# Kernel optimization log

Measured on AMD Instinct MI355X. Metric: run time of the kernel, lower is better.

The kernel has to match this reference:

```python
import jax, jax.numpy as jnp
import numpy as np

N = 50000
E = 800000
D_IN = 128
D_OUT = 128


def setup_inputs() -> dict:
    key = jax.random.key(0)
    ks = jax.random.split(key, 12)
    x = jax.random.normal(ks[0], (N, D_IN), dtype=jnp.float32)
    edge_index = jax.random.randint(ks[1], (2, E), 0, N, dtype=jnp.int64)
    importance = jax.random.uniform(ks[2], (N, 1), dtype=jnp.float32)
    s = 1.0 / np.sqrt(D_IN)
    W_msg = jax.random.uniform(ks[3], (D_IN, D_OUT), jnp.float32, -s, s)
    b_msg = jax.random.uniform(ks[4], (D_OUT,), jnp.float32, -s, s)
    s2 = 1.0 / np.sqrt(D_IN + D_OUT)
    W_upd = jax.random.uniform(ks[5], (D_IN + D_OUT, D_OUT), jnp.float32, -s2, s2)
    b_upd = jax.random.uniform(ks[6], (D_OUT,), jnp.float32, -s2, s2)
    s3 = 1.0 / np.sqrt(D_OUT + 1)
    W_gate = jax.random.uniform(ks[7], (D_OUT + 1, D_OUT), jnp.float32, -s3, s3)
    b_gate = jax.random.uniform(ks[8], (D_OUT,), jnp.float32, -s3, s3)
    s4 = 1.0 / np.sqrt(D_OUT)
    W_imp = jax.random.uniform(ks[9], (D_OUT, 1), jnp.float32, -s4, s4)
    b_imp = jax.random.uniform(ks[10], (1,), jnp.float32, -s4, s4)
    return {
        "x": x, "edge_index": edge_index, "importance": importance,
        "W_msg": W_msg, "b_msg": b_msg, "W_upd": W_upd, "b_upd": b_upd,
        "W_gate": W_gate, "b_gate": b_gate, "W_imp": W_imp, "b_imp": b_imp,
    }


def reference(x, edge_index, importance, W_msg, b_msg, W_upd, b_upd,
              W_gate, b_gate, W_imp, b_imp):
    src, dst = edge_index[0], edge_index[1]
    # message: lin_message(x_j). Transform nodes once (N < E), then gather.
    m_nodes = x @ W_msg + b_msg              # [N, D_OUT]
    msgs = m_nodes[src]                      # [E, D_OUT] gather
    aggr = jax.ops.segment_sum(msgs, dst, num_segments=N)  # [N, D_OUT] scatter-add
    # update: lin_update(cat([x, aggr]))
    conv_out = jnp.concatenate([x, aggr], axis=-1) @ W_upd + b_upd  # [N, D_OUT]
    # sigmoid-gated residual mix with importance
    gate_in = jnp.concatenate([conv_out, importance], axis=-1)      # [N, D_OUT+1]
    gate = jax.nn.sigmoid(gate_in @ W_gate + b_gate)
    out = gate * conv_out + (1.0 - gate) * x
    propagated_importance = out @ W_imp + b_imp                     # [N, 1]
    return out, propagated_importance
```

## Files before the change

kernel.cpp:

```cpp
#include <hip/hip_runtime.h>
#include <hip/hip_bf16.h>

#define D 128
#define BR 64
#define PWS 132
#define PXS 65

__global__ void count_deg(const int* __restrict__ ei, int* __restrict__ deg, int E) {
    int e = blockIdx.x * 256 + threadIdx.x;
    if (e < E) atomicAdd(&deg[ei[E + e]], 1);
}

__global__ __launch_bounds__(256) void scan_kernel(const int* __restrict__ deg,
                                                   int* __restrict__ rowstart,
                                                   int* __restrict__ cursor, int n) {
    __shared__ int tsum[257];
    int tid = threadIdx.x;
    int chunk = (n + 255) / 256;
    int lo = tid * chunk;
    int hi = lo + chunk; if (hi > n) hi = n;
    int s = 0;
    for (int i = lo; i < hi; ++i) s += deg[i];
    tsum[tid] = s;
    __syncthreads();
    if (tid == 0) {
        int run = 0;
        for (int i = 0; i < 256; ++i) { int t = tsum[i]; tsum[i] = run; run += t; }
        tsum[256] = run;
    }
    __syncthreads();
    int run = tsum[tid];
    for (int i = lo; i < hi; ++i) {
        rowstart[i] = run; cursor[i] = run; run += deg[i];
    }
    if (tid == 0) rowstart[n] = tsum[256];
}

__global__ void fill_csr(const int* __restrict__ ei, int* __restrict__ cursor,
                         int* __restrict__ csr, int E) {
    int e = blockIdx.x * 256 + threadIdx.x;
    if (e < E) {
        int s = ei[e];
        int d = ei[E + e];
        int p = atomicAdd(&cursor[d], 1);
        csr[p] = s;
    }
}

__global__ __launch_bounds__(256, 3) void gemm_msg(const float* __restrict__ x,
                                                   const float* __restrict__ W,
                                                   const float* __restrict__ b,
                                                   float* __restrict__ out, int n) {
    __shared__ __align__(16) float Ws[64 * PWS];
    __shared__ __align__(16) float Xs[BR * PXS];
    const int tid = threadIdx.x;
    const int R0 = blockIdx.x * BR;
    const int tr = tid >> 5, tc = tid & 31;
    const int r0 = tr * 8, c0 = tc * 4;

    float acc[8][4];
#pragma unroll
    for (int i = 0; i < 8; ++i)
#pragma unroll
        for (int j = 0; j < 4; ++j) acc[i][j] = 0.f;

    for (int ch = 0; ch < 2; ++ch) {
        const int k0 = ch * 64;
        if (ch) __syncthreads();
        for (int t = 0; t < 32; ++t) {
            int e = t * 256 + tid;
            int k = e >> 7, c = e & 127;
            Ws[k * PWS + c] = W[(k0 + k) * D + c];
        }
        for (int t = 0; t < 16; ++t) {
            int e = t * 256 + tid;
            int r = e >> 6, c = e & 63;
            int gr = R0 + r; if (gr >= n) gr = n - 1;
            Xs[r * PXS + c] = x[(long)gr * D + k0 + c];
        }
        __syncthreads();
        for (int k = 0; k < 64; ++k) {
            float4 wa = *(const float4*)&Ws[k * PWS + c0];
            float xs[8];
#pragma unroll
            for (int i = 0; i < 8; ++i) xs[i] = Xs[(r0 + i) * PXS + k];
#pragma unroll
            for (int i = 0; i < 8; ++i) {
                acc[i][0] += xs[i] * wa.x; acc[i][1] += xs[i] * wa.y;
                acc[i][2] += xs[i] * wa.z; acc[i][3] += xs[i] * wa.w;
            }
        }
    }

    const float4 bj = *(const float4*)&b[c0];
#pragma unroll
    for (int i = 0; i < 8; ++i) {
        int row = R0 + r0 + i;
        if (row < n) {
            float4 o;
            o.x = acc[i][0] + bj.x; o.y = acc[i][1] + bj.y;
            o.z = acc[i][2] + bj.z; o.w = acc[i][3] + bj.w;
            *(float4*)&out[(long)row * D + c0] = o;
        }
    }
}

__global__ __launch_bounds__(256) void aggr_kernel(const float* __restrict__ mn,
                                                   const int* __restrict__ rowstart,
                                                   const int* __restrict__ csr,
                                                   float* __restrict__ aggr, int n) {
    int gw = (blockIdx.x * 256 + threadIdx.x) >> 6;
    int lane = threadIdx.x & 63;
    if (gw >= n) return;
    int rs = rowstart[gw], re = rowstart[gw + 1];
    float ax = 0.f, ay = 0.f, bx = 0.f, by = 0.f;
    int i = rs;
    for (; i + 1 < re; i += 2) {
        int s0 = csr[i], s1 = csr[i + 1];
        float2 v0 = *(const float2*)&mn[(long)s0 * D + lane * 2];
        float2 v1 = *(const float2*)&mn[(long)s1 * D + lane * 2];
        ax += v0.x; ay += v0.y; bx += v1.x; by += v1.y;
    }
    if (i < re) {
        int s0 = csr[i];
        float2 v0 = *(const float2*)&mn[(long)s0 * D + lane * 2];
        ax += v0.x; ay += v0.y;
    }
    float2 o; o.x = ax + bx; o.y = ay + by;
    *(float2*)&aggr[(long)gw * D + lane * 2] = o;
}

__global__ __launch_bounds__(256, 3) void fused_update(
        const float* __restrict__ x, const float* __restrict__ aggr,
        const float* __restrict__ imp,
        const float* __restrict__ W_upd, const float* __restrict__ b_upd,
        const float* __restrict__ W_gate, const float* __restrict__ b_gate,
        const float* __restrict__ W_imp, const float* __restrict__ b_imp,
        float* __restrict__ out, int n) {
    __shared__ __align__(16) float Ws[64 * PWS];
    __shared__ __align__(16) float Xs[BR * PXS];
    const int tid = threadIdx.x;
    const int R0 = blockIdx.x * BR;
    const int tr = tid >> 5, tc = tid & 31;
    const int r0 = tr * 8, c0 = tc * 4;

    float acc[8][4];
#pragma unroll
    for (int i = 0; i < 8; ++i)
#pragma unroll
        for (int j = 0; j < 4; ++j) acc[i][j] = 0.f;

    for (int ch = 0; ch < 4; ++ch) {
        const int k0 = ch * 64;
        const float* src = (ch < 2) ? x : aggr;
        const int koff = (ch & 1) * 64;
        if (ch) __syncthreads();
        for (int t = 0; t < 32; ++t) {
            int e = t * 256 + tid;
            int k = e >> 7, c = e & 127;
            Ws[k * PWS + c] = W_upd[(k0 + k) * D + c];
        }
        for (int t = 0; t < 16; ++t) {
            int e = t * 256 + tid;
            int r = e >> 6, c = e & 63;
            int gr = R0 + r; if (gr >= n) gr = n - 1;
            Xs[r * PXS + c] = src[(long)gr * D + koff + c];
        }
        __syncthreads();
        for (int k = 0; k < 64; ++k) {
            float4 wa = *(const float4*)&Ws[k * PWS + c0];
            float xs[8];
#pragma unroll
            for (int i = 0; i < 8; ++i) xs[i] = Xs[(r0 + i) * PXS + k];
#pragma unroll
            for (int i = 0; i < 8; ++i) {
                acc[i][0] += xs[i] * wa.x; acc[i][1] += xs[i] * wa.y;
                acc[i][2] += xs[i] * wa.z; acc[i][3] += xs[i] * wa.w;
            }
        }
    }

    {
        const float4 bu = *(const float4*)&b_upd[c0];
#pragma unroll
        for (int i = 0; i < 8; ++i) {
            acc[i][0] += bu.x; acc[i][1] += bu.y;
            acc[i][2] += bu.z; acc[i][3] += bu.w;
        }
    }

    float g[8][4];
#pragma unroll
    for (int i = 0; i < 8; ++i)
#pragma unroll
        for (int j = 0; j < 4; ++j) g[i][j] = 0.f;

    for (int gc = 0; gc < 2; ++gc) {
        __syncthreads();
        for (int t = 0; t < 32; ++t) {
            int e = t * 256 + tid;
            int k = e >> 7, c = e & 127;
            Ws[k * PWS + c] = W_gate[(gc * 64 + k) * D + c];
        }
        if ((c0 >> 6) == gc) {
            const int cb = c0 & 63;
#pragma unroll
            for (int i = 0; i < 8; ++i)
#pragma unroll
                for (int j = 0; j < 4; ++j)
                    Xs[(r0 + i) * PXS + cb + j] = acc[i][j];
        }
        __syncthreads();
        for (int k = 0; k < 64; ++k) {
            float4 wa = *(const float4*)&Ws[k * PWS + c0];
            float xs[8];
#pragma unroll
            for (int i = 0; i < 8; ++i) xs[i] = Xs[(r0 + i) * PXS + k];
#pragma unroll
            for (int i = 0; i < 8; ++i) {
                g[i][0] += xs[i] * wa.x; g[i][1] += xs[i] * wa.y;
                g[i][2] += xs[i] * wa.z; g[i][3] += xs[i] * wa.w;
            }
        }
    }

    const float4 wgl = *(const float4*)&W_gate[128 * D + c0];
    const float4 bg  = *(const float4*)&b_gate[c0];
    const float4 wim = *(const float4*)&W_imp[c0];
    const float bi = b_imp[0];

#pragma unroll
    for (int i = 0; i < 8; ++i) {
        int row = R0 + r0 + i;
        int crow = row < n ? row : n - 1;
        float iv = imp[crow];
        float4 xv = *(const float4*)&x[(long)crow * D + c0];
        float z0 = g[i][0] + iv * wgl.x + bg.x;
        float z1 = g[i][1] + iv * wgl.y + bg.y;
        float z2 = g[i][2] + iv * wgl.z + bg.z;
        float z3 = g[i][3] + iv * wgl.w + bg.w;
        float s0 = 1.0f / (1.0f + expf(-z0));
        float s1 = 1.0f / (1.0f + expf(-z1));
        float s2 = 1.0f / (1.0f + expf(-z2));
        float s3 = 1.0f / (1.0f + expf(-z3));
        g[i][0] = s0 * acc[i][0] + (1.0f - s0) * xv.x;
        g[i][1] = s1 * acc[i][1] + (1.0f - s1) * xv.y;
        g[i][2] = s2 * acc[i][2] + (1.0f - s2) * xv.z;
        g[i][3] = s3 * acc[i][3] + (1.0f - s3) * xv.w;
        if (row < n) {
            float4 o; o.x = g[i][0]; o.y = g[i][1]; o.z = g[i][2]; o.w = g[i][3];
            *(float4*)&out[(long)row * D + c0] = o;
        }
    }

#pragma unroll
    for (int i = 0; i < 8; ++i) {
        float pi = g[i][0] * wim.x + g[i][1] * wim.y + g[i][2] * wim.z + g[i][3] * wim.w;
#pragma unroll
        for (int m = 16; m >= 1; m >>= 1) pi += __shfl_xor(pi, m, 32);
        int row = R0 + r0 + i;
        if (tc == 0 && row < n) out[(long)n * D + row] = pi + bi;
    }
}

extern "C" void kernel_launch(void* const* d_in, const int* in_sizes, int n_in,
                              void* d_out, int out_size, void* d_ws, size_t ws_size,
                              hipStream_t stream) {
    const float* x      = (const float*)d_in[0];
    const int*   ei     = (const int*)d_in[1];
    const float* imp    = (const float*)d_in[2];
    const float* W_msg  = (const float*)d_in[3];
    const float* b_msg  = (const float*)d_in[4];
    const float* W_upd  = (const float*)d_in[5];
    const float* b_upd  = (const float*)d_in[6];
    const float* W_gate = (const float*)d_in[7];
    const float* b_gate = (const float*)d_in[8];
    const float* W_imp  = (const float*)d_in[9];
    const float* b_imp  = (const float*)d_in[10];
    float* out = (float*)d_out;

    const int N = in_sizes[0] / D;
    const int E = in_sizes[1] / 2;

    char* ws = (char*)d_ws;
    float* m_nodes  = (float*)ws;  ws += (size_t)N * D * sizeof(float);
    float* aggr     = (float*)ws;  ws += (size_t)N * D * sizeof(float);
    int*   deg      = (int*)ws;    ws += (size_t)N * sizeof(int);
    int*   rowstart = (int*)ws;    ws += (size_t)(N + 1) * sizeof(int);
    int*   cursor   = (int*)ws;    ws += (size_t)N * sizeof(int);
    int*   csr      = (int*)ws;    ws += (size_t)E * sizeof(int);

    hipMemsetAsync(deg, 0, (size_t)N * sizeof(int), stream);

    count_deg<<<(E + 255) / 256, 256, 0, stream>>>(ei, deg, E);
    scan_kernel<<<1, 256, 0, stream>>>(deg, rowstart, cursor, N);
    fill_csr<<<(E + 255) / 256, 256, 0, stream>>>(ei, cursor, csr, E);

    const int nblk = (N + BR - 1) / BR;
    gemm_msg<<<nblk, 256, 0, stream>>>(x, W_msg, b_msg, m_nodes, N);

    aggr_kernel<<<((size_t)N * 64 + 255) / 256, 256, 0, stream>>>(
        m_nodes, rowstart, csr, aggr, N);

    fused_update<<<nblk, 256, 0, stream>>>(x, aggr, imp, W_upd, b_upd,
                                           W_gate, b_gate, W_imp, b_imp,
                                           out, N);
}
```

Measured before the change: 649.7 us.

## Use 256-row register-blocked GEMM tiles and split fused update into two kernels

Result: slower. 666.6 us (+2.6%).

```diff
diff --git a/kernel.cpp b/kernel.cpp
--- a/kernel.cpp
+++ b/kernel.cpp
@@ -2,9 +2,10 @@
 #include <hip/hip_bf16.h>
 
 #define D 128
-#define BR 64
-#define PWS 132
-#define PXS 65
+#define BRF 256
+#define KC 32
+#define PWT 132
+#define PXT 260
 
 __global__ void count_deg(const int* __restrict__ ei, int* __restrict__ deg, int E) {
     int e = blockIdx.x * 256 + threadIdx.x;
@@ -47,61 +48,245 @@
     }
 }
 
-__global__ __launch_bounds__(256, 3) void gemm_msg(const float* __restrict__ x,
-                                                   const float* __restrict__ W,
-                                                   const float* __restrict__ b,
-                                                   float* __restrict__ out, int n) {
-    __shared__ __align__(16) float Ws[64 * PWS];
-    __shared__ __align__(16) float Xs[BR * PXS];
+
+__global__ __launch_bounds__(256) void gemm128(const float* __restrict__ src,
+                                               const float* __restrict__ W,
+                                               const float* __restrict__ b,
+                                               float* __restrict__ out, int n) {
+    __shared__ __align__(16) float Ws[KC * PWT];
+    __shared__ __align__(16) float XsT[KC * PXT];
     const int tid = threadIdx.x;
-    const int R0 = blockIdx.x * BR;
-    const int tr = tid >> 5, tc = tid & 31;
-    const int r0 = tr * 8, c0 = tc * 4;
-
-    float acc[8][4];
-#pragma unroll
-    for (int i = 0; i < 8; ++i)
-#pragma unroll
-        for (int j = 0; j < 4; ++j) acc[i][j] = 0.f;
-
-    for (int ch = 0; ch < 2; ++ch) {
-        const int k0 = ch * 64;
+    const int R0 = blockIdx.x * BRF;
+    const int tr = tid >> 4, tc = tid & 15;
+    const int r0 = tr * 16, c0a = tc * 4, c0b = 64 + tc * 4;
+
+    float acc[16][8];
+#pragma unroll
+    for (int i = 0; i < 16; ++i)
+#pragma unroll
+        for (int j = 0; j < 8; ++j) acc[i][j] = 0.f;
+
+    for (int ch = 0; ch < 4; ++ch) {
+        const int k0 = ch * KC;
         if (ch) __syncthreads();
+#pragma unroll
+        for (int t = 0; t < 16; ++t) {
+            int e = t * 256 + tid;
+            int k = e >> 7, c = e & 127;
+            Ws[k * PWT + c] = W[(k0 + k) * D + c];
+        }
+#pragma unroll
         for (int t = 0; t < 32; ++t) {
             int e = t * 256 + tid;
-            int k = e >> 7, c = e & 127;
-            Ws[k * PWS + c] = W[(k0 + k) * D + c];
-        }
-        for (int t = 0; t < 16; ++t) {
-            int e = t * 256 + tid;
-            int r = e >> 6, c = e & 63;
+            int c = e & 31, r = e >> 5;
             int gr = R0 + r; if (gr >= n) gr = n - 1;
-            Xs[r * PXS + c] = x[(long)gr * D + k0 + c];
+            XsT[c * PXT + r] = src[(long)gr * D + k0 + c];
         }
         __syncthreads();
-        for (int k = 0; k < 64; ++k) {
-            float4 wa = *(const float4*)&Ws[k * PWS + c0];
-            float xs[8];
-#pragma unroll
-            for (int i = 0; i < 8; ++i) xs[i] = Xs[(r0 + i) * PXS + k];
-#pragma unroll
-            for (int i = 0; i < 8; ++i) {
+        for (int k = 0; k < KC; ++k) {
+            float xs[16];
+            *(float4*)&xs[0]  = *(const float4*)&XsT[k * PXT + r0];
+            *(float4*)&xs[4]  = *(const float4*)&XsT[k * PXT + r0 + 4];
+            *(float4*)&xs[8]  = *(const float4*)&XsT[k * PXT + r0 + 8];
+            *(float4*)&xs[12] = *(const float4*)&XsT[k * PXT + r0 + 12];
+            float4 wa = *(const float4*)&Ws[k * PWT + c0a];
+            float4 wb = *(const float4*)&Ws[k * PWT + c0b];
+#pragma unroll
+            for (int i = 0; i < 16; ++i) {
                 acc[i][0] += xs[i] * wa.x; acc[i][1] += xs[i] * wa.y;
                 acc[i][2] += xs[i] * wa.z; acc[i][3] += xs[i] * wa.w;
+                acc[i][4] += xs[i] * wb.x; acc[i][5] += xs[i] * wb.y;
+                acc[i][6] += xs[i] * wb.z; acc[i][7] += xs[i] * wb.w;
             }
         }
     }
 
-    const float4 bj = *(const float4*)&b[c0];
-#pragma unroll
-    for (int i = 0; i < 8; ++i) {
+    const float4 ba = *(const float4*)&b[c0a];
+    const float4 bb = *(const float4*)&b[c0b];
+#pragma unroll
+    for (int i = 0; i < 16; ++i) {
         int row = R0 + r0 + i;
         if (row < n) {
-            float4 o;
-            o.x = acc[i][0] + bj.x; o.y = acc[i][1] + bj.y;
-            o.z = acc[i][2] + bj.z; o.w = acc[i][3] + bj.w;
-            *(float4*)&out[(long)row * D + c0] = o;
-        }
+            float4 o0, o1;
+            o0.x = acc[i][0] + ba.x; o0.y = acc[i][1] + ba.y;
+            o0.z = acc[i][2] + ba.z; o0.w = acc[i][3] + ba.w;
+            o1.x = acc[i][4] + bb.x; o1.y = acc[i][5] + bb.y;
+            o1.z = acc[i][6] + bb.z; o1.w = acc[i][7] + bb.w;
+            *(float4*)&out[(long)row * D + c0a] = o0;
+            *(float4*)&out[(long)row * D + c0b] = o1;
+        }
+    }
+}
+
+__global__ __launch_bounds__(256) void gemm_upd(const float* __restrict__ x,
+                                                const float* __restrict__ aggr,
+                                                const float* __restrict__ W,
+                                                const float* __restrict__ b,
+                                                float* __restrict__ out, int n) {
+    __shared__ __align__(16) float Ws[KC * PWT];
+    __shared__ __align__(16) float XsT[KC * PXT];
+    const int tid = threadIdx.x;
+    const int R0 = blockIdx.x * BRF;
+    const int tr = tid >> 4, tc = tid & 15;
+    const int r0 = tr * 16, c0a = tc * 4, c0b = 64 + tc * 4;
+
+    float acc[16][8];
+#pragma unroll
+    for (int i = 0; i < 16; ++i)
+#pragma unroll
+        for (int j = 0; j < 8; ++j) acc[i][j] = 0.f;
+
+    for (int ch = 0; ch < 8; ++ch) {
+        const int k0 = ch * KC;
+        const float* src = (ch < 4) ? x : aggr;
+        const int koff = (ch & 3) * KC;
+        if (ch) __syncthreads();
+#pragma unroll
+        for (int t = 0; t < 16; ++t) {
+            int e = t * 256 + tid;
+            int k = e >> 7, c = e & 127;
+            Ws[k * PWT + c] = W[(k0 + k) * D + c];
+        }
+#pragma unroll
+        for (int t = 0; t < 32; ++t) {
+            int e = t * 256 + tid;
+            int c = e & 31, r = e >> 5;
+            int gr = R0 + r; if (gr >= n) gr = n - 1;
+            XsT[c * PXT + r] = src[(long)gr * D + koff + c];
+        }
+        __syncthreads();
+        for (int k = 0; k < KC; ++k) {
+            float xs[16];
+            *(float4*)&xs[0]  = *(const float4*)&XsT[k * PXT + r0];
+            *(float4*)&xs[4]  = *(const float4*)&XsT[k * PXT + r0 + 4];
+            *(float4*)&xs[8]  = *(const float4*)&XsT[k * PXT + r0 + 8];
+            *(float4*)&xs[12] = *(const float4*)&XsT[k * PXT + r0 + 12];
+            float4 wa = *(const float4*)&Ws[k * PWT + c0a];
+            float4 wb = *(const float4*)&Ws[k * PWT + c0b];
+#pragma unroll
+            for (int i = 0; i < 16; ++i) {
+                acc[i][0] += xs[i] * wa.x; acc[i][1] += xs[i] * wa.y;
+                acc[i][2] += xs[i] * wa.z; acc[i][3] += xs[i] * wa.w;
+                acc[i][4] += xs[i] * wb.x; acc[i][5] += xs[i] * wb.y;
+                acc[i][6] += xs[i] * wb.z; acc[i][7] += xs[i] * wb.w;
+            }
+        }
+    }
+
+    const float4 ba = *(const float4*)&b[c0a];
+    const float4 bb = *(const float4*)&b[c0b];
+#pragma unroll
+    for (int i = 0; i < 16; ++i) {
+        int row = R0 + r0 + i;
+        if (row < n) {
+            float4 o0, o1;
+            o0.x = acc[i][0] + ba.x; o0.y = acc[i][1] + ba.y;
+            o0.z = acc[i][2] + ba.z; o0.w = acc[i][3] + ba.w;
+            o1.x = acc[i][4] + bb.x; o1.y = acc[i][5] + bb.y;
+            o1.z = acc[i][6] + bb.z; o1.w = acc[i][7] + bb.w;
+            *(float4*)&out[(long)row * D + c0a] = o0;
+            *(float4*)&out[(long)row * D + c0b] = o1;
+        }
+    }
+}
+
+__global__ __launch_bounds__(256) void gate_mix(const float* __restrict__ conv,
+                                                const float* __restrict__ x,
+                                                const float* __restrict__ imp,
+                                                const float* __restrict__ Wg,
+                                                const float* __restrict__ bg,
+                                                const float* __restrict__ Wi,
+                                                const float* __restrict__ bi_p,
+                                                float* __restrict__ out, int n) {
+    __shared__ __align__(16) float Ws[KC * PWT];
+    __shared__ __align__(16) float XsT[KC * PXT];
+    const int tid = threadIdx.x;
+    const int R0 = blockIdx.x * BRF;
+    const int tr = tid >> 4, tc = tid & 15;
+    const int r0 = tr * 16, c0a = tc * 4, c0b = 64 + tc * 4;
+
+    float acc[16][8];
+#pragma unroll
+    for (int i = 0; i < 16; ++i)
+#pragma unroll
+        for (int j = 0; j < 8; ++j) acc[i][j] = 0.f;
+
+    for (int ch = 0; ch < 4; ++ch) {
+        const int k0 = ch * KC;
+        if (ch) __syncthreads();
+#pragma unroll
+        for (int t = 0; t < 16; ++t) {
+            int e = t * 256 + tid;
+            int k = e >> 7, c = e & 127;
+            Ws[k * PWT + c] = Wg[(k0 + k) * D + c];
+        }
+#pragma unroll
+        for (int t = 0; t < 32; ++t) {
+            int e = t * 256 + tid;
+            int c = e & 31, r = e >> 5;
+            int gr = R0 + r; if (gr >= n) gr = n - 1;
+            XsT[c * PXT + r] = conv[(long)gr * D + k0 + c];
+        }
+        __syncthreads();
+        for (int k = 0; k < KC; ++k) {
+            float xs[16];
+            *(float4*)&xs[0]  = *(const float4*)&XsT[k * PXT + r0];
+            *(float4*)&xs[4]  = *(const float4*)&XsT[k * PXT + r0 + 4];
+            *(float4*)&xs[8]  = *(const float4*)&XsT[k * PXT + r0 + 8];
+            *(float4*)&xs[12] = *(const float4*)&XsT[k * PXT + r0 + 12];
+            float4 wa = *(const float4*)&Ws[k * PWT + c0a];
+            float4 wb = *(const float4*)&Ws[k * PWT + c0b];
+#pragma unroll
+            for (int i = 0; i < 16; ++i) {
+                acc[i][0] += xs[i] * wa.x; acc[i][1] += xs[i] * wa.y;
+                acc[i][2] += xs[i] * wa.z; acc[i][3] += xs[i] * wa.w;
+                acc[i][4] += xs[i] * wb.x; acc[i][5] += xs[i] * wb.y;
+                acc[i][6] += xs[i] * wb.z; acc[i][7] += xs[i] * wb.w;
+            }
+        }
+    }
+
+    const float4 wga = *(const float4*)&Wg[128 * D + c0a];
+    const float4 wgb = *(const float4*)&Wg[128 * D + c0b];
+    const float4 bga = *(const float4*)&bg[c0a];
+    const float4 bgb = *(const float4*)&bg[c0b];
+    const float4 wia = *(const float4*)&Wi[c0a];
+    const float4 wib = *(const float4*)&Wi[c0b];
+    const float bi = bi_p[0];
+
+#pragma unroll
+    for (int i = 0; i < 16; ++i) {
+        int row = R0 + r0 + i;
+        int crow = row < n ? row : n - 1;
+        float iv = imp[crow];
+        float4 cva = *(const float4*)&conv[(long)crow * D + c0a];
+        float4 cvb = *(const float4*)&conv[(long)crow * D + c0b];
+        float4 xva = *(const float4*)&x[(long)crow * D + c0a];
+        float4 xvb = *(const float4*)&x[(long)crow * D + c0b];
+
+        float z, s;
+        z = acc[i][0] + iv * wga.x + bga.x; s = 1.f/(1.f+expf(-z)); acc[i][0] = s*cva.x + (1.f-s)*xva.x;
+        z = acc[i][1] + iv * wga.y + bga.y; s = 1.f/(1.f+expf(-z)); acc[i][1] = s*cva.y + (1.f-s)*xva.y;
+        z = acc[i][2] + iv * wga.z + bga.z; s = 1.f/(1.f+expf(-z)); acc[i][2] = s*cva.z + (1.f-s)*xva.z;
+        z = acc[i][3] + iv * wga.w + bga.w; s = 1.f/(1.f+expf(-z)); acc[i][3] = s*cva.w + (1.f-s)*xva.w;
+        z = acc[i][4] + iv * wgb.x + bgb.x; s = 1.f/(1.f+expf(-z)); acc[i][4] = s*cvb.x + (1.f-s)*xvb.x;
+        z = acc[i][5] + iv * wgb.y + bgb.y; s = 1.f/(1.f+expf(-z)); acc[i][5] = s*cvb.y + (1.f-s)*xvb.y;
+        z = acc[i][6] + iv * wgb.z + bgb.z; s = 1.f/(1.f+expf(-z)); acc[i][6] = s*cvb.z + (1.f-s)*xvb.z;
+        z = acc[i][7] + iv * wgb.w + bgb.w; s = 1.f/(1.f+expf(-z)); acc[i][7] = s*cvb.w + (1.f-s)*xvb.w;
+
+        if (row < n) {
+            float4 o0, o1;
+            o0.x = acc[i][0]; o0.y = acc[i][1]; o0.z = acc[i][2]; o0.w = acc[i][3];
+            o1.x = acc[i][4]; o1.y = acc[i][5]; o1.z = acc[i][6]; o1.w = acc[i][7];
+            *(float4*)&out[(long)row * D + c0a] = o0;
+            *(float4*)&out[(long)row * D + c0b] = o1;
+        }
+
+        float pi = acc[i][0]*wia.x + acc[i][1]*wia.y + acc[i][2]*wia.z + acc[i][3]*wia.w
+                 + acc[i][4]*wib.x + acc[i][5]*wib.y + acc[i][6]*wib.z + acc[i][7]*wib.w;
+#pragma unroll
+        for (int m = 8; m >= 1; m >>= 1) pi += __shfl_xor(pi, m, 16);
+        if (tc == 0 && row < n) out[(long)n * D + row] = pi + bi;
     }
 }
 
@@ -113,154 +298,24 @@
     int lane = threadIdx.x & 63;
     if (gw >= n) return;
     int rs = rowstart[gw], re = rowstart[gw + 1];
-    float ax = 0.f, ay = 0.f, bx = 0.f, by = 0.f;
+    float a0x=0.f,a0y=0.f,a1x=0.f,a1y=0.f,a2x=0.f,a2y=0.f,a3x=0.f,a3y=0.f;
     int i = rs;
-    for (; i + 1 < re; i += 2) {
-        int s0 = csr[i], s1 = csr[i + 1];
+    for (; i + 3 < re; i += 4) {
+        int s0 = csr[i], s1 = csr[i+1], s2 = csr[i+2], s3 = csr[i+3];
         float2 v0 = *(const float2*)&mn[(long)s0 * D + lane * 2];
         float2 v1 = *(const float2*)&mn[(long)s1 * D + lane * 2];
-        ax += v0.x; ay += v0.y; bx += v1.x; by += v1.y;
-    }
-    if (i < re) {
+        float2 v2 = *(const float2*)&mn[(long)s2 * D + lane * 2];
+        float2 v3 = *(const float2*)&mn[(long)s3 * D + lane * 2];
+        a0x += v0.x; a0y += v0.y; a1x += v1.x; a1y += v1.y;
+        a2x += v2.x; a2y += v2.y; a3x += v3.x; a3y += v3.y;
+    }
+    for (; i < re; ++i) {
         int s0 = csr[i];
         float2 v0 = *(const float2*)&mn[(long)s0 * D + lane * 2];
-        ax += v0.x; ay += v0.y;
-    }
-    float2 o; o.x = ax + bx; o.y = ay + by;
+        a0x += v0.x; a0y += v0.y;
+    }
+    float2 o; o.x = (a0x + a1x) + (a2x + a3x); o.y = (a0y + a1y) + (a2y + a3y);
     *(float2*)&aggr[(long)gw * D + lane * 2] = o;
-}
-
-__global__ __launch_bounds__(256, 3) void fused_update(
-        const float* __restrict__ x, const float* __restrict__ aggr,
-        const float* __restrict__ imp,
-        const float* __restrict__ W_upd, const float* __restrict__ b_upd,
-        const float* __restrict__ W_gate, const float* __restrict__ b_gate,
-        const float* __restrict__ W_imp, const float* __restrict__ b_imp,
-        float* __restrict__ out, int n) {
-    __shared__ __align__(16) float Ws[64 * PWS];
-    __shared__ __align__(16) float Xs[BR * PXS];
-    const int tid = threadIdx.x;
-    const int R0 = blockIdx.x * BR;
-    const int tr = tid >> 5, tc = tid & 31;
-    const int r0 = tr * 8, c0 = tc * 4;
-
-    float acc[8][4];
-#pragma unroll
-    for (int i = 0; i < 8; ++i)
-#pragma unroll
-        for (int j = 0; j < 4; ++j) acc[i][j] = 0.f;
-
-    for (int ch = 0; ch < 4; ++ch) {
-        const int k0 = ch * 64;
-        const float* src = (ch < 2) ? x : aggr;
-        const int koff = (ch & 1) * 64;
-        if (ch) __syncthreads();
-        for (int t = 0; t < 32; ++t) {
-            int e = t * 256 + tid;
-            int k = e >> 7, c = e & 127;
-            Ws[k * PWS + c] = W_upd[(k0 + k) * D + c];
-        }
-        for (int t = 0; t < 16; ++t) {
-            int e = t * 256 + tid;
-            int r = e >> 6, c = e & 63;
-            int gr = R0 + r; if (gr >= n) gr = n - 1;
-            Xs[r * PXS + c] = src[(long)gr * D + koff + c];
-        }
-        __syncthreads();
-        for (int k = 0; k < 64; ++k) {
-            float4 wa = *(const float4*)&Ws[k * PWS + c0];
-            float xs[8];
-#pragma unroll
-            for (int i = 0; i < 8; ++i) xs[i] = Xs[(r0 + i) * PXS + k];
-#pragma unroll
-            for (int i = 0; i < 8; ++i) {
-                acc[i][0] += xs[i] * wa.x; acc[i][1] += xs[i] * wa.y;
-                acc[i][2] += xs[i] * wa.z; acc[i][3] += xs[i] * wa.w;
-            }
-        }
-    }
-
-    {
-        const float4 bu = *(const float4*)&b_upd[c0];
-#pragma unroll
-        for (int i = 0; i < 8; ++i) {
-            acc[i][0] += bu.x; acc[i][1] += bu.y;
-            acc[i][2] += bu.z; acc[i][3] += bu.w;
-        }
-    }
-
-    float g[8][4];
-#pragma unroll
-    for (int i = 0; i < 8; ++i)
-#pragma unroll
-        for (int j = 0; j < 4; ++j) g[i][j] = 0.f;
-
-    for (int gc = 0; gc < 2; ++gc) {
-        __syncthreads();
-        for (int t = 0; t < 32; ++t) {
-            int e = t * 256 + tid;
-            int k = e >> 7, c = e & 127;
-            Ws[k * PWS + c] = W_gate[(gc * 64 + k) * D + c];
-        }
-        if ((c0 >> 6) == gc) {
-            const int cb = c0 & 63;
-#pragma unroll
-            for (int i = 0; i < 8; ++i)
-#pragma unroll
-                for (int j = 0; j < 4; ++j)
-                    Xs[(r0 + i) * PXS + cb + j] = acc[i][j];
-        }
-        __syncthreads();
-        for (int k = 0; k < 64; ++k) {
-            float4 wa = *(const float4*)&Ws[k * PWS + c0];
-            float xs[8];
-#pragma unroll
-            for (int i = 0; i < 8; ++i) xs[i] = Xs[(r0 + i) * PXS + k];
-#pragma unroll
-            for (int i = 0; i < 8; ++i) {
-                g[i][0] += xs[i] * wa.x; g[i][1] += xs[i] * wa.y;
-                g[i][2] += xs[i] * wa.z; g[i][3] += xs[i] * wa.w;
-            }
-        }
-    }
-
-    const float4 wgl = *(const float4*)&W_gate[128 * D + c0];
-    const float4 bg  = *(const float4*)&b_gate[c0];
-    const float4 wim = *(const float4*)&W_imp[c0];
-    const float bi = b_imp[0];
-
-#pragma unroll
-    for (int i = 0; i < 8; ++i) {
-        int row = R0 + r0 + i;
-        int crow = row < n ? row : n - 1;
-        float iv = imp[crow];
-        float4 xv = *(const float4*)&x[(long)crow * D + c0];
-        float z0 = g[i][0] + iv * wgl.x + bg.x;
-        float z1 = g[i][1] + iv * wgl.y + bg.y;
-        float z2 = g[i][2] + iv * wgl.z + bg.z;
-        float z3 = g[i][3] + iv * wgl.w + bg.w;
-        float s0 = 1.0f / (1.0f + expf(-z0));
-        float s1 = 1.0f / (1.0f + expf(-z1));
-        float s2 = 1.0f / (1.0f + expf(-z2));
-        float s3 = 1.0f / (1.0f + expf(-z3));
-        g[i][0] = s0 * acc[i][0] + (1.0f - s0) * xv.x;
-        g[i][1] = s1 * acc[i][1] + (1.0f - s1) * xv.y;
-        g[i][2] = s2 * acc[i][2] + (1.0f - s2) * xv.z;
-        g[i][3] = s3 * acc[i][3] + (1.0f - s3) * xv.w;
-        if (row < n) {
-            float4 o; o.x = g[i][0]; o.y = g[i][1]; o.z = g[i][2]; o.w = g[i][3];
-            *(float4*)&out[(long)row * D + c0] = o;
-        }
-    }
-
-#pragma unroll
-    for (int i = 0; i < 8; ++i) {
-        float pi = g[i][0] * wim.x + g[i][1] * wim.y + g[i][2] * wim.z + g[i][3] * wim.w;
-#pragma unroll
-        for (int m = 16; m >= 1; m >>= 1) pi += __shfl_xor(pi, m, 32);
-        int row = R0 + r0 + i;
-        if (tc == 0 && row < n) out[(long)n * D + row] = pi + bi;
-    }
 }
 
 extern "C" void kernel_launch(void* const* d_in, const int* in_sizes, int n_in,
@@ -296,13 +351,15 @@
     scan_kernel<<<1, 256, 0, stream>>>(deg, rowstart, cursor, N);
     fill_csr<<<(E + 255) / 256, 256, 0, stream>>>(ei, cursor, csr, E);
 
-    const int nblk = (N + BR - 1) / BR;
-    gemm_msg<<<nblk, 256, 0, stream>>>(x, W_msg, b_msg, m_nodes, N);
+    const int nblk = (N + BRF - 1) / BRF;
+    gemm128<<<nblk, 256, 0, stream>>>(x, W_msg, b_msg, m_nodes, N);
 
     aggr_kernel<<<((size_t)N * 64 + 255) / 256, 256, 0, stream>>>(
         m_nodes, rowstart, csr, aggr, N);
 
-    fused_update<<<nblk, 256, 0, stream>>>(x, aggr, imp, W_upd, b_upd,
-                                           W_gate, b_gate, W_imp, b_imp,
-                                           out, N);
-}
+    float* conv = m_nodes;
+    gemm_upd<<<nblk, 256, 0, stream>>>(x, aggr, W_upd, b_upd, conv, N);
+
+    gate_mix<<<nblk, 256, 0, stream>>>(conv, x, imp, W_gate, b_gate,
+                                       W_imp, b_imp, out, N);
+}
```
